# Optimization experiments

Measured on AMD Instinct MI355X. Metric: run time of the kernel, lower is better.

The kernel has to match this reference:

```python
import jax, jax.numpy as jnp
import numpy as np

# All 8 VTM downsampling filter sets in the source are identical; one 16x12 table.
FILTER = np.array([
    [0,0,0,0,0,128,0,0,0,0,0,0],
    [0,0,0,2,-6,127,7,-2,0,0,0,0],
    [0,0,0,3,-12,125,16,-5,1,0,0,0],
    [0,0,0,4,-16,120,26,-7,1,0,0,0],
    [0,0,0,5,-18,114,36,-10,1,0,0,0],
    [0,0,0,5,-20,107,46,-12,2,0,0,0],
    [0,0,0,5,-21,99,57,-15,3,0,0,0],
    [0,0,0,5,-20,89,68,-18,4,0,0,0],
    [0,0,0,4,-19,79,79,-19,4,0,0,0],
    [0,0,0,4,-18,68,89,-20,5,0,0,0],
    [0,0,0,3,-15,57,99,-21,5,0,0,0],
    [0,0,0,2,-12,46,107,-20,5,0,0,0],
    [0,0,0,1,-10,36,114,-18,5,0,0,0],
    [0,0,0,1,-7,26,120,-16,4,0,0,0],
    [0,0,0,1,-5,16,125,-12,3,0,0,0],
    [0,0,0,0,-2,7,127,-6,2,0,0,0],
], dtype=np.float32)

BIT_DEPTH = 8
MAX_VAL = (1 << BIT_DEPTH) - 1  # 255
SCALING_RATIO = int(2.0 * (1 << 14))  # 32768 for scale_factor=2.0 -> filter idx 3 (all identical)


def _phase_params(n_out):
    # ref_pos = (i << 1) * scaling_ratio >> 14 ; integer = ref_pos >> 4 ; frac = ref_pos & 15
    i = np.arange(n_out, dtype=np.int64)
    ref = ((i << 1) * SCALING_RATIO) >> 14
    integer = (ref >> 4).astype(np.int32)
    frac = (ref & 15).astype(np.int32)
    return integer, frac


def setup_inputs() -> dict:
    key = jax.random.key(0)
    # integer-valued pixels in [0, 255], stored as float32 (as the torch module consumes)
    x = jax.random.randint(key, (8, 3, 1080, 1920), 0, 256).astype(jnp.float32)
    return {"x": x}


def reference(x) -> jnp.ndarray:
    B, C, H, W = x.shape
    Wo, Ho = W // 2, H // 2

    # ---- horizontal pass ----
    xi, xf = _phase_params(Wo)
    cx = jnp.asarray(FILTER[xf])  # (Wo, 12) phase-selected coeffs
    buf = jnp.zeros((B, C, H, Wo), dtype=jnp.float32)
    for k in range(12):  # fixed 12-tap loop; data dims fully vectorized
        idx = np.clip(xi + k - 5, 0, W - 1)  # integer + k - 6 + 1, edge-clamped
        buf = buf + cx[:, k] * x[..., idx]
    # torch stores the float sum into an int32 buffer -> truncation toward zero
    buf = jnp.trunc(buf)

    # ---- vertical pass ----
    yi, yf = _phase_params(Ho)
    cy = jnp.asarray(FILTER[yf])  # (Ho, 12)
    acc = jnp.zeros((B, C, Ho, Wo), dtype=jnp.float32)
    for k in range(12):
        idy = np.clip(yi + k - 5, 0, H - 1)
        acc = acc + cy[:, k][:, None] * buf[:, :, idy, :]

    # (sum + (1<<13)) >> 14 on int32 == floor((sum + 8192)/16384); exact in fp32 (<2^24)
    normalized = jnp.floor((acc + 8192.0) * (1.0 / 16384.0))
    return jnp.clip(normalized, 0.0, float(MAX_VAL))
```

## Files before the change

### kernel.cpp

```cpp
#include <hip/hip_runtime.h>


#define H_IN   1080
#define W_IN   1920
#define H_OUT  540
#define W_OUT  960
#define N_BC   24

__global__ __launch_bounds__(256)
void vtm_down_kernel(const float* __restrict__ x, float* __restrict__ out)
{
    const int tx = blockIdx.x * 64 + threadIdx.x;
    if (tx >= W_OUT / 4) return;
    const int yo = blockIdx.y * 4 + threadIdx.y;
    const int bc = blockIdx.z;

    const int xi = tx;
    const int yi = yo >> 2;
    const int yp = yo & 3;

    const float P0[6] = {0.f, 0.f, 128.f, 0.f, 0.f, 0.f};
    const float P1[6] = {5.f, -18.f, 114.f, 36.f, -10.f, 1.f};
    const float P2[6] = {4.f, -19.f, 79.f, 79.f, -19.f, 4.f};
    const float P3[6] = {1.f, -10.f, 36.f, 114.f, -18.f, 5.f};

    const float* __restrict__ xb = x + (size_t)bc * (H_IN * W_IN);

    float v[6] = {0.f, 0.f, 0.f, 0.f, 0.f, 0.f};
    #pragma unroll
    for (int s = 0; s < 6; ++s) {
        int r = yi - 2 + s;
        r = r < 0 ? 0 : r;
        const float cys = (yp == 0) ? P0[s] : (yp == 1) ? P1[s]
                        : (yp == 2) ? P2[s] : P3[s];
        const float* __restrict__ row = xb + (size_t)r * W_IN;
        #pragma unroll
        for (int t = 0; t < 6; ++t) {
            int c = xi - 2 + t;
            c = c < 0 ? 0 : c;
            v[t] += cys * row[c];
        }
    }

    float a0 = 128.f * v[2];
    float a1 = 5.f*v[0] - 18.f*v[1] + 114.f*v[2] +  36.f*v[3] - 10.f*v[4] + 1.f*v[5];
    float a2 = 4.f*v[0] - 19.f*v[1] +  79.f*v[2] +  79.f*v[3] - 19.f*v[4] + 4.f*v[5];
    float a3 = 1.f*v[0] - 10.f*v[1] +  36.f*v[2] + 114.f*v[3] - 18.f*v[4] + 5.f*v[5];

    const float k = 1.f / 16384.f;
    float4 o;
    o.x = fminf(fmaxf(floorf((a0 + 8192.f) * k), 0.f), 255.f);
    o.y = fminf(fmaxf(floorf((a1 + 8192.f) * k), 0.f), 255.f);
    o.z = fminf(fmaxf(floorf((a2 + 8192.f) * k), 0.f), 255.f);
    o.w = fminf(fmaxf(floorf((a3 + 8192.f) * k), 0.f), 255.f);

    float* __restrict__ op = out + ((size_t)bc * H_OUT + yo) * W_OUT + 4 * tx;
    *reinterpret_cast<float4*>(op) = o;
}

extern "C" void kernel_launch(void* const* d_in, const int* in_sizes, int n_in,
                              void* d_out, int out_size, void* d_ws, size_t ws_size,
                              hipStream_t stream)
{
    const float* x = (const float*)d_in[0];
    float* out = (float*)d_out;

    dim3 block(64, 4, 1);
    dim3 grid(4 , H_OUT / 4, N_BC);
    hipLaunchKernelGGL(vtm_down_kernel, grid, block, 0, stream, x, out);
}
```

Baseline: 254.3 us.

## Stage input tile in LDS and compute four output rows per thread

Each block now loads a 9x69 input tile into shared memory once, and each thread computes all four vertical phases (four output rows) from the same six input rows held in registers, writing each row with a nontemporal store. This removes repeated global loads of overlapping input rows and columns across threads. The grid shrinks to 34 row-blocks, which raises per-thread register use and adds a block-wide sync. Bounds checks guard the last partial block.

```diff
diff --git a/kernel.cpp b/kernel.cpp
--- a/kernel.cpp
+++ b/kernel.cpp
@@ -6,56 +6,85 @@
 #define H_OUT  540
 #define W_OUT  960
 #define N_BC   24
+#define XI_N   (W_OUT/4)
+#define YI_N   (H_OUT/4)
+
+#define TILE_R 9
+#define TILE_C 69
+#define TILE_CP 72
+
+typedef float v4f __attribute__((ext_vector_type(4)));
 
 __global__ __launch_bounds__(256)
 void vtm_down_kernel(const float* __restrict__ x, float* __restrict__ out)
 {
-    const int tx = blockIdx.x * 64 + threadIdx.x;
-    if (tx >= W_OUT / 4) return;
-    const int yo = blockIdx.y * 4 + threadIdx.y;
-    const int bc = blockIdx.z;
-
-    const int xi = tx;
-    const int yi = yo >> 2;
-    const int yp = yo & 3;
-
-    const float P0[6] = {0.f, 0.f, 128.f, 0.f, 0.f, 0.f};
-    const float P1[6] = {5.f, -18.f, 114.f, 36.f, -10.f, 1.f};
-    const float P2[6] = {4.f, -19.f, 79.f, 79.f, -19.f, 4.f};
-    const float P3[6] = {1.f, -10.f, 36.f, 114.f, -18.f, 5.f};
+    const int lane = threadIdx.x;
+    const int ty   = threadIdx.y;
+    const int bx   = blockIdx.x;
+    const int by   = blockIdx.y;
+    const int bc   = blockIdx.z;
 
     const float* __restrict__ xb = x + (size_t)bc * (H_IN * W_IN);
 
-    float v[6] = {0.f, 0.f, 0.f, 0.f, 0.f, 0.f};
+    __shared__ float tile[TILE_R][TILE_CP];
+
+    const int r0 = 4 * by - 2;
+    const int c0 = 64 * bx - 2;
+    #pragma unroll
+    for (int r = ty; r < TILE_R; r += 4) {
+        int gr = r0 + r; gr = gr < 0 ? 0 : gr;
+        const float* __restrict__ row = xb + (size_t)gr * W_IN;
+        for (int c = lane; c < TILE_C; c += 64) {
+            int gc = c0 + c; gc = gc < 0 ? 0 : gc;
+            tile[r][c] = row[gc];
+        }
+    }
+    __syncthreads();
+
+    const int xi = bx * 64 + lane;
+    const int yi = by * 4 + ty;
+    if (xi >= XI_N || yi >= YI_N) return;
+
+    const float C1[6] = {5.f, -18.f, 114.f, 36.f, -10.f, 1.f};
+    const float C2[6] = {4.f, -19.f,  79.f, 79.f, -19.f, 4.f};
+    const float C3[6] = {1.f, -10.f,  36.f,114.f, -18.f, 5.f};
+
+    float v0[6], v1[6] = {0,0,0,0,0,0}, v2[6] = {0,0,0,0,0,0}, v3[6] = {0,0,0,0,0,0};
     #pragma unroll
     for (int s = 0; s < 6; ++s) {
-        int r = yi - 2 + s;
-        r = r < 0 ? 0 : r;
-        const float cys = (yp == 0) ? P0[s] : (yp == 1) ? P1[s]
-                        : (yp == 2) ? P2[s] : P3[s];
-        const float* __restrict__ row = xb + (size_t)r * W_IN;
+        float w[6];
+        #pragma unroll
+        for (int t = 0; t < 6; ++t) w[t] = tile[ty + s][lane + t];
+        if (s == 2) {
+            #pragma unroll
+            for (int t = 0; t < 6; ++t) v0[t] = 128.f * w[t];
+        }
         #pragma unroll
         for (int t = 0; t < 6; ++t) {
-            int c = xi - 2 + t;
-            c = c < 0 ? 0 : c;
-            v[t] += cys * row[c];
+            v1[t] = fmaf(C1[s], w[t], v1[t]);
+            v2[t] = fmaf(C2[s], w[t], v2[t]);
+            v3[t] = fmaf(C3[s], w[t], v3[t]);
         }
     }
 
-    float a0 = 128.f * v[2];
-    float a1 = 5.f*v[0] - 18.f*v[1] + 114.f*v[2] +  36.f*v[3] - 10.f*v[4] + 1.f*v[5];
-    float a2 = 4.f*v[0] - 19.f*v[1] +  79.f*v[2] +  79.f*v[3] - 19.f*v[4] + 4.f*v[5];
-    float a3 = 1.f*v[0] - 10.f*v[1] +  36.f*v[2] + 114.f*v[3] - 18.f*v[4] + 5.f*v[5];
+    const float k = 1.f / 16384.f;
+    float* __restrict__ ob = out + ((size_t)bc * H_OUT + 4 * yi) * W_OUT + 4 * xi;
 
-    const float k = 1.f / 16384.f;
-    float4 o;
-    o.x = fminf(fmaxf(floorf((a0 + 8192.f) * k), 0.f), 255.f);
-    o.y = fminf(fmaxf(floorf((a1 + 8192.f) * k), 0.f), 255.f);
-    o.z = fminf(fmaxf(floorf((a2 + 8192.f) * k), 0.f), 255.f);
-    o.w = fminf(fmaxf(floorf((a3 + 8192.f) * k), 0.f), 255.f);
+    #pragma unroll
+    for (int p = 0; p < 4; ++p) {
+        const float* v = (p == 0) ? v0 : (p == 1) ? v1 : (p == 2) ? v2 : v3;
+        float a0 = 128.f * v[2];
+        float a1 = 5.f*v[0] - 18.f*v[1] + 114.f*v[2] +  36.f*v[3] - 10.f*v[4] + 1.f*v[5];
+        float a2 = 4.f*v[0] - 19.f*v[1] +  79.f*v[2] +  79.f*v[3] - 19.f*v[4] + 4.f*v[5];
+        float a3 = 1.f*v[0] - 10.f*v[1] +  36.f*v[2] + 114.f*v[3] - 18.f*v[4] + 5.f*v[5];
 
-    float* __restrict__ op = out + ((size_t)bc * H_OUT + yo) * W_OUT + 4 * tx;
-    *reinterpret_cast<float4*>(op) = o;
+        v4f o;
+        o.x = fminf(fmaxf(floorf((a0 + 8192.f) * k), 0.f), 255.f);
+        o.y = fminf(fmaxf(floorf((a1 + 8192.f) * k), 0.f), 255.f);
+        o.z = fminf(fmaxf(floorf((a2 + 8192.f) * k), 0.f), 255.f);
+        o.w = fminf(fmaxf(floorf((a3 + 8192.f) * k), 0.f), 255.f);
+        __builtin_nontemporal_store(o, reinterpret_cast<v4f*>(ob + (size_t)p * W_OUT));
+    }
 }
 
 extern "C" void kernel_launch(void* const* d_in, const int* in_sizes, int n_in,
@@ -66,6 +95,6 @@
     float* out = (float*)d_out;
 
     dim3 block(64, 4, 1);
-    dim3 grid(4 , H_OUT / 4, N_BC);
+    dim3 grid(4 , 34 , N_BC);
     hipLaunchKernelGGL(vtm_down_kernel, grid, block, 0, stream, x, out);
 }
```

New measurement: 241.3 us. -5.1%, faster.
